# Kernel optimization log

Hardware: AMD Instinct MI355X
Metric: run time of the kernel (lower is better)

## Reference

```python
import jax, jax.numpy as jnp
import numpy as np

N = 100000      # number of nodes (z rows) and z0 rows
E = 1000000     # number of edges
EMB = 128       # args.emb_size


def setup_inputs() -> dict:
    key = jax.random.key(0)
    k1, k2, k3, k4, k5 = jax.random.split(key, 5)
    z = jax.random.normal(k1, (N, EMB), dtype=jnp.float32)
    z0 = jax.random.normal(k2, (N, EMB), dtype=jnp.float32)
    edge_index = jax.random.randint(k3, (2, E), 0, N, dtype=jnp.int64)
    # torch Linear weights: [out_features, in_features]
    Wq = jax.random.normal(k4, (EMB, 2 * EMB), dtype=jnp.float32) * (1.0 / np.sqrt(2 * EMB))
    Wo = jax.random.normal(k5, (1, 2 * EMB), dtype=jnp.float32) * (1.0 / np.sqrt(2 * EMB))
    bo = jnp.zeros((1,), dtype=jnp.float32)
    return {"z": z, "edge_index": edge_index, "z0": z0, "Wq": Wq, "Wo": Wo, "bo": bo}


def reference(z, edge_index, z0, Wq, Wo, bo):
    # qid: per-edge max of the two endpoint ids, shifted to start at 0
    qid = jnp.max(edge_index[0:2], axis=0)
    qid = qid - qid.min()
    emb1 = z[edge_index[0]]            # [E, EMB]
    emb2 = z[edge_index[1]]            # [E, EMB]
    x0 = jnp.concatenate([emb2, z0[qid]], axis=-1) @ Wq.T   # [E, EMB]
    out = jnp.concatenate([emb1, x0], axis=-1) @ Wo.T + bo  # [E, 1]
    return out.reshape(-1)
```

## Files before the change

kernel.cpp:

```cpp
#include <hip/hip_runtime.h>
#include <climits>

#define EMB 128
#define EMB2 256
#define QBLOCKS 512

typedef float v4f __attribute__((ext_vector_type(4)));
typedef int   v4i __attribute__((ext_vector_type(4)));

__global__ void prep_kernel(const float* __restrict__ Wq,
                            const float* __restrict__ Wo,
                            const int* __restrict__ ei, int E,
                            float* __restrict__ weff,
                            int* __restrict__ slots) {
    if (blockIdx.x == 0) {
        int k = threadIdx.x;
        float acc = 0.f;
#pragma unroll 8
        for (int j = 0; j < EMB; ++j)
            acc += Wo[EMB + j] * Wq[j * EMB2 + k];
        weff[k] = acc;
        return;
    }
    int m = INT_MAX;
    int nvec = E >> 2;
    int nthreads = QBLOCKS * blockDim.x;
    int tid = (blockIdx.x - 1) * blockDim.x + threadIdx.x;
    const v4i* r0 = (const v4i*)ei;
    const v4i* r1 = (const v4i*)(ei + E);
    for (int v = tid; v < nvec; v += nthreads) {
        v4i a = r0[v];
        v4i b = r1[v];
        int m0 = max(a.x, b.x), m1 = max(a.y, b.y);
        int m2 = max(a.z, b.z), m3 = max(a.w, b.w);
        m = min(m, min(min(m0, m1), min(m2, m3)));
    }
    if (blockIdx.x == 1 && threadIdx.x < (E & 3)) {
        int e = (nvec << 2) + threadIdx.x;
        m = min(m, max(ei[e], ei[e + E]));
    }
#pragma unroll
    for (int off = 32; off; off >>= 1)
        m = min(m, __shfl_xor(m, off, 64));
    __shared__ int sm[4];
    int wid = threadIdx.x >> 6;
    if ((threadIdx.x & 63) == 0) sm[wid] = m;
    __syncthreads();
    if (threadIdx.x == 0)
        slots[blockIdx.x - 1] = min(min(sm[0], sm[1]), min(sm[2], sm[3]));
}

__global__ void node_dots_kernel(const float* __restrict__ z,
                                 const float* __restrict__ z0,
                                 const float* __restrict__ Wo,
                                 const float* __restrict__ weff,
                                 v4f* __restrict__ tab,
                                 int N) {
    int gtid = blockIdx.x * blockDim.x + threadIdx.x;
    int wave = gtid >> 6;
    int lane = gtid & 63;
    int sub = lane >> 5;
    int c = lane & 31;
    int row = wave * 2 + sub;
    if (row >= N) return;

    v4f w1 = ((const v4f*)Wo)[c];
    v4f wa = ((const v4f*)weff)[c];
    v4f wb = ((const v4f*)weff)[32 + c];

    v4f zv  = __builtin_nontemporal_load(((const v4f*)(z  + (size_t)row * EMB)) + c);
    v4f z0v = __builtin_nontemporal_load(((const v4f*)(z0 + (size_t)row * EMB)) + c);

    float p1 = w1.x * zv.x + w1.y * zv.y + w1.z * zv.z + w1.w * zv.w;
    float p2 = wa.x * zv.x + wa.y * zv.y + wa.z * zv.z + wa.w * zv.w;
    float p3 = wb.x * z0v.x + wb.y * z0v.y + wb.z * z0v.z + wb.w * z0v.w;

#pragma unroll
    for (int off = 16; off; off >>= 1) {
        p1 += __shfl_xor(p1, off, 64);
        p2 += __shfl_xor(p2, off, 64);
        p3 += __shfl_xor(p3, off, 64);
    }
    if (c == 0) {
        v4f r; r.x = p1; r.y = p2; r.z = p3; r.w = 0.f;
        tab[row] = r;
    }
}

__global__ void edge_out_kernel(const int* __restrict__ ei,
                                const v4f* __restrict__ tab,
                                const int* __restrict__ slots,
                                const float* __restrict__ bo,
                                float* __restrict__ out, int E) {
    __shared__ int sq[5];
    {
        int t = threadIdx.x;
        int mm = min(slots[t], slots[t + 256]);
#pragma unroll
        for (int off = 32; off; off >>= 1)
            mm = min(mm, __shfl_xor(mm, off, 64));
        if ((t & 63) == 0) sq[t >> 6] = mm;
        __syncthreads();
        if (t == 0) sq[4] = min(min(sq[0], sq[1]), min(sq[2], sq[3]));
        __syncthreads();
    }
    const int qmin = sq[4];
    const float b0 = *bo;

    int t = blockIdx.x * blockDim.x + threadIdx.x;
    int e4 = t << 2;
    if (e4 + 3 < E) {
        v4i a = *(const v4i*)(ei + e4);
        v4i b = *(const v4i*)(ei + E + e4);
        v4f r;
        r.x = tab[a.x].x + tab[b.x].y + tab[max(a.x, b.x) - qmin].z + b0;
        r.y = tab[a.y].x + tab[b.y].y + tab[max(a.y, b.y) - qmin].z + b0;
        r.z = tab[a.z].x + tab[b.z].y + tab[max(a.z, b.z) - qmin].z + b0;
        r.w = tab[a.w].x + tab[b.w].y + tab[max(a.w, b.w) - qmin].z + b0;
        __builtin_nontemporal_store(r, (v4f*)(out + e4));
    } else {
        for (int e = e4; e < E; ++e) {
            int a = ei[e], b = ei[e + E];
            out[e] = tab[a].x + tab[b].y + tab[max(a, b) - qmin].z + b0;
        }
    }
}

extern "C" void kernel_launch(void* const* d_in, const int* in_sizes, int n_in,
                              void* d_out, int out_size, void* d_ws, size_t ws_size,
                              hipStream_t stream) {
    const float* z    = (const float*)d_in[0];
    const int*   ei   = (const int*)d_in[1];
    const float* z0   = (const float*)d_in[2];
    const float* Wq   = (const float*)d_in[3];
    const float* Wo   = (const float*)d_in[4];
    const float* bo   = (const float*)d_in[5];
    float* out = (float*)d_out;

    int N = in_sizes[0] / EMB;
    int E = in_sizes[1] / 2;

    v4f* tab = (v4f*)d_ws;
    float* weff = (float*)(tab + N);
    int* slots = (int*)(weff + EMB2);

    prep_kernel<<<1 + QBLOCKS, 256, 0, stream>>>(Wq, Wo, ei, E, weff, slots);

    int pairs = (N + 1) / 2;
    int blocksC = (pairs + 3) / 4;
    node_dots_kernel<<<blocksC, 256, 0, stream>>>(z, z0, Wo, weff, tab, N);

    int threadsD = (E + 3) / 4;
    int blocksD = (threadsD + 255) / 256;
    edge_out_kernel<<<blocksD, 256, 0, stream>>>(ei, tab, slots, bo, out, E);
}
```

Before: 153.2 us.

## Fold the qid term into per-node table so each edge needs two gathers

Each node's table entry now holds the z0 projection for row-qmin already added to its z dot products, as extra lanes p1+p3 and p2+p3. The edge kernel picks lanes based on which endpoint is larger. That needs two scalar gathers per edge instead of three, and the qmin reduction moves into the node kernel. The node kernel now does that reduction in every block and reads z0 at a shifted row, trading extra per-node work for fewer random reads per edge.

New measurement: 152.6 us. Within noise of the previous version (-0.4%).

```diff
diff --git a/kernel.cpp b/kernel.cpp
--- a/kernel.cpp
+++ b/kernel.cpp
@@ -54,8 +54,23 @@
                                  const float* __restrict__ z0,
                                  const float* __restrict__ Wo,
                                  const float* __restrict__ weff,
+                                 const int* __restrict__ slots,
                                  v4f* __restrict__ tab,
                                  int N) {
+    __shared__ int sq[5];
+    {
+        int t = threadIdx.x;
+        int mm = min(slots[t], slots[t + 256]);
+#pragma unroll
+        for (int off = 32; off; off >>= 1)
+            mm = min(mm, __shfl_xor(mm, off, 64));
+        if ((t & 63) == 0) sq[t >> 6] = mm;
+        __syncthreads();
+        if (t == 0) sq[4] = min(min(sq[0], sq[1]), min(sq[2], sq[3]));
+        __syncthreads();
+    }
+    const int qmin = sq[4];
+
     int gtid = blockIdx.x * blockDim.x + threadIdx.x;
     int wave = gtid >> 6;
     int lane = gtid & 63;
@@ -69,11 +84,15 @@
     v4f wb = ((const v4f*)weff)[32 + c];
 
     v4f zv  = __builtin_nontemporal_load(((const v4f*)(z  + (size_t)row * EMB)) + c);
-    v4f z0v = __builtin_nontemporal_load(((const v4f*)(z0 + (size_t)row * EMB)) + c);
 
     float p1 = w1.x * zv.x + w1.y * zv.y + w1.z * zv.z + w1.w * zv.w;
     float p2 = wa.x * zv.x + wa.y * zv.y + wa.z * zv.z + wa.w * zv.w;
-    float p3 = wb.x * z0v.x + wb.y * z0v.y + wb.z * z0v.z + wb.w * z0v.w;
+    float p3 = 0.f;
+    int zr = row - qmin;
+    if (zr >= 0) {
+        v4f z0v = __builtin_nontemporal_load(((const v4f*)(z0 + (size_t)zr * EMB)) + c);
+        p3 = wb.x * z0v.x + wb.y * z0v.y + wb.z * z0v.z + wb.w * z0v.w;
+    }
 
 #pragma unroll
     for (int off = 16; off; off >>= 1) {
@@ -82,46 +101,44 @@
         p3 += __shfl_xor(p3, off, 64);
     }
     if (c == 0) {
-        v4f r; r.x = p1; r.y = p2; r.z = p3; r.w = 0.f;
+        v4f r; r.x = p1; r.y = p2; r.z = p1 + p3; r.w = p2 + p3;
         tab[row] = r;
     }
 }
 
 __global__ void edge_out_kernel(const int* __restrict__ ei,
-                                const v4f* __restrict__ tab,
-                                const int* __restrict__ slots,
+                                const float* __restrict__ qt,
                                 const float* __restrict__ bo,
                                 float* __restrict__ out, int E) {
-    __shared__ int sq[5];
-    {
-        int t = threadIdx.x;
-        int mm = min(slots[t], slots[t + 256]);
-#pragma unroll
-        for (int off = 32; off; off >>= 1)
-            mm = min(mm, __shfl_xor(mm, off, 64));
-        if ((t & 63) == 0) sq[t >> 6] = mm;
-        __syncthreads();
-        if (t == 0) sq[4] = min(min(sq[0], sq[1]), min(sq[2], sq[3]));
-        __syncthreads();
-    }
-    const int qmin = sq[4];
     const float b0 = *bo;
-
     int t = blockIdx.x * blockDim.x + threadIdx.x;
     int e4 = t << 2;
     if (e4 + 3 < E) {
         v4i a = *(const v4i*)(ei + e4);
         v4i b = *(const v4i*)(ei + E + e4);
         v4f r;
-        r.x = tab[a.x].x + tab[b.x].y + tab[max(a.x, b.x) - qmin].z + b0;
-        r.y = tab[a.y].x + tab[b.y].y + tab[max(a.y, b.y) - qmin].z + b0;
-        r.z = tab[a.z].x + tab[b.z].y + tab[max(a.z, b.z) - qmin].z + b0;
-        r.w = tab[a.w].x + tab[b.w].y + tab[max(a.w, b.w) - qmin].z + b0;
+        {
+            int g = (a.x >= b.x);
+            r.x = qt[(a.x << 2) | (g ? 2 : 0)] + qt[(b.x << 2) | (g ? 1 : 3)] + b0;
+        }
+        {
+            int g = (a.y >= b.y);
+            r.y = qt[(a.y << 2) | (g ? 2 : 0)] + qt[(b.y << 2) | (g ? 1 : 3)] + b0;
+        }
+        {
+            int g = (a.z >= b.z);
+            r.z = qt[(a.z << 2) | (g ? 2 : 0)] + qt[(b.z << 2) | (g ? 1 : 3)] + b0;
+        }
+        {
+            int g = (a.w >= b.w);
+            r.w = qt[(a.w << 2) | (g ? 2 : 0)] + qt[(b.w << 2) | (g ? 1 : 3)] + b0;
+        }
         __builtin_nontemporal_store(r, (v4f*)(out + e4));
     } else {
         for (int e = e4; e < E; ++e) {
             int a = ei[e], b = ei[e + E];
-            out[e] = tab[a].x + tab[b].y + tab[max(a, b) - qmin].z + b0;
+            int g = (a >= b);
+            out[e] = qt[(a << 2) | (g ? 2 : 0)] + qt[(b << 2) | (g ? 1 : 3)] + b0;
         }
     }
 }
@@ -148,9 +165,9 @@
 
     int pairs = (N + 1) / 2;
     int blocksC = (pairs + 3) / 4;
-    node_dots_kernel<<<blocksC, 256, 0, stream>>>(z, z0, Wo, weff, tab, N);
+    node_dots_kernel<<<blocksC, 256, 0, stream>>>(z, z0, Wo, weff, slots, tab, N);
 
     int threadsD = (E + 3) / 4;
     int blocksD = (threadsD + 255) / 256;
-    edge_out_kernel<<<blocksD, 256, 0, stream>>>(ei, tab, slots, bo, out, E);
+    edge_out_kernel<<<blocksD, 256, 0, stream>>>(ei, (const float*)tab, bo, out, E);
 }
```
